# Optimization experiments

Measured on AMD Instinct MI355X. Metric: run time of the kernel, lower is better.

## Reference

```python
import jax, jax.numpy as jnp
import numpy as np

IM = 128  # imSize
BZ = 32


def setup_inputs() -> dict:
    key = jax.random.key(0)
    k1, k2 = jax.random.split(key)
    return {
        "input": jax.random.normal(k1, (BZ, 2, IM, IM), dtype=jnp.float32),
        "mask": jax.random.uniform(k2, (BZ, 1, 1, IM), dtype=jnp.float32),  # unused by forward (as in the torch code)
    }


def _kspace_map(x):
    # x: [B, H, W] real image.
    # Torch pipeline: K = FFT2(x) (unnormalized, torch.rfft onesided=False);
    # for each column i, zero out all k-space columns except i, then IFFT2
    # (normalized=False -> includes 1/(H*W)) and keep the real part.
    # Because each masked spectrum has a single nonzero column, IFFT2 factors:
    #   sep[b,i,u,v] = (1/W) * Re( t[b,u,i] * exp(2j*pi*i*v/W) ),
    # where t = IFFT_rows(K) (includes 1/H). Same math, no (B*W,H,W) FFTs.
    B, H, W = x.shape
    K = jnp.fft.fft2(x)                      # [B,H,W] complex, unnormalized fwd FFT
    t = jnp.fft.ifft(K, axis=1)              # ifft over rows -> carries the 1/H factor
    tt = jnp.transpose(t, (0, 2, 1))         # [B, i(col), u]
    v = jnp.arange(W, dtype=x.dtype)
    ang = (2.0 * np.pi / W) * (v[:, None] * v[None, :])   # [i, v]
    cos_t, sin_t = jnp.cos(ang), jnp.sin(ang)
    # Re(t * e^{j*ang}) = Re(t)*cos - Im(t)*sin  (avoids a large complex temp)
    sep = (tt.real[:, :, :, None] * cos_t[:, None, :]
           - tt.imag[:, :, :, None] * sin_t[:, None, :]) / W   # [B, W, H, W]
    return sep.astype(x.dtype)


def reference(input, mask):
    x = input[:, 0, :, :]          # first channel -> image used for k-space map
    others = input[:, 1:, :, :]    # remaining channels passed through
    sep = _kspace_map(x)           # [B, imSize, H, W]
    return jnp.concatenate([sep, others], axis=1)
```

## Files before the change

kernel.cpp:

```cpp
#include <hip/hip_runtime.h>
#include <math.h>

#define IM 128
#define BZ 32

typedef float v4f __attribute__((ext_vector_type(4)));

__global__ __launch_bounds__(256) void kspace_kernel(const float* __restrict__ in,
                                                     float* __restrict__ out) {
    const int row = blockIdx.x;
    const int b   = row >> 7;
    const int h   = row & (IM - 1);
    const int tid = threadIdx.x;

    const float A = 6.28318530717958647692f / (float)IM;

    __shared__ float xr[IM];
    __shared__ float tre[IM];
    __shared__ float tim[IM];

    const float* xrow = in + (((size_t)b * 2 + 0) * IM + h) * IM;
    if (tid < IM) xr[tid] = xrow[tid];
    __syncthreads();

    {
        const int v     = tid >> 1;
        const int part  = tid & 1;
        const int wbase = part << 6;

        float pc, ps;
        { int k = (v * wbase) & (IM - 1); sincosf(A * (float)k, &ps, &pc); ps = -ps; }
        float rc, rs;
        sincosf(A * (float)v, &rs, &rc); rs = -rs;

        float sre = 0.0f, sim = 0.0f;
        #pragma unroll 8
        for (int i = 0; i < 64; ++i) {
            const float xv = xr[wbase + i];
            sre = fmaf(xv, pc, sre);
            sim = fmaf(xv, ps, sim);
            const float npc = pc * rc - ps * rs;
            ps = fmaf(ps, rc, pc * rs);
            pc = npc;
        }
        sre += __shfl_xor(sre, 1);
        sim += __shfl_xor(sim, 1);
        if (part == 0) {
            tre[v] = sre * (1.0f / IM);
            tim[v] = sim * (1.0f / IM);
        }
    }
    __syncthreads();

    float* outb = out + (size_t)b * 129 * IM * IM + (size_t)h * IM;
    const int vsub = tid >> 5;
    const int w0   = (tid & 31) * 4;

    float pc, ps;
    { int k = (vsub * w0) & (IM - 1); sincosf(A * (float)k, &ps, &pc); }
    float rc, rs;
    sincosf(A * (float)vsub, &rs, &rc);
    float wc, ws;
    { int k = (8 * w0) & (IM - 1); sincosf(A * (float)k, &ws, &wc); }
    const float sc = 0.92387953251128675613f;
    const float ss = 0.38268343236508977173f;

    #pragma unroll
    for (int it = 0; it < 16; ++it) {
        const int v = it * 8 + vsub;
        const float re = tre[v];
        const float im = tim[v];

        v4f r;
        float c = pc, s = ps;
        r.x = re * c - im * s;
        float nc = c * rc - s * rs; s = fmaf(s, rc, c * rs); c = nc;
        r.y = re * c - im * s;
        nc = c * rc - s * rs; s = fmaf(s, rc, c * rs); c = nc;
        r.z = re * c - im * s;
        nc = c * rc - s * rs; s = fmaf(s, rc, c * rs); c = nc;
        r.w = re * c - im * s;
        *(v4f*)(outb + (size_t)v * IM * IM + w0) = r;

        nc = pc * wc - ps * ws; ps = fmaf(ps, wc, pc * ws); pc = nc;
        nc = rc * sc - rs * ss; rs = fmaf(rs, sc, rc * ss); rc = nc;
    }

    if (tid < 32) {
        const v4f* src = (const v4f*)(in + (((size_t)b * 2 + 1) * IM + h) * IM);
        v4f*       dst = (v4f*)(out + (((size_t)b * 129 + 128) * IM + h) * IM);
        dst[tid] = src[tid];
    }
}

extern "C" void kernel_launch(void* const* d_in, const int* in_sizes, int n_in,
                              void* d_out, int out_size, void* d_ws, size_t ws_size,
                              hipStream_t stream) {
    const float* in = (const float*)d_in[0];
    float* out = (float*)d_out;
    kspace_kernel<<<dim3(BZ * IM), dim3(256), 0, stream>>>(in, out);
}
```

Baseline: 273.9 us.

## Split into DFT and emit kernels, staging row DFT results in output buffer

Splits the single kernel in two. The first computes the per-row DFT and stages the real and imaginary parts in the first two rows of each output plane. The second launches one block per (column plane, batch), reads the staged values and writes the whole contiguous 64KB plane using a shared-memory twiddle table instead of recurrences. The goal is contiguous large writes per block in place of scattered 512B row writes, at the cost of a second launch and an extra global round trip. The emit kernel overwrites the staging rows it reads, which is safe only because all threads load them into shared memory before the barrier.

```diff
diff --git a/kernel.cpp b/kernel.cpp
--- a/kernel.cpp
+++ b/kernel.cpp
@@ -6,9 +6,11 @@
 
 typedef float v4f __attribute__((ext_vector_type(4)));
 
-__global__ __launch_bounds__(256) void kspace_kernel(const float* __restrict__ in,
-                                                     float* __restrict__ out) {
-    const int row = blockIdx.x;
+
+__global__ __launch_bounds__(256) void dft_kernel(const float* __restrict__ in,
+                                                  float* __restrict__ out) {
+    const int g   = blockIdx.x;
+    const int row = (g & 7) * (BZ * IM / 8) + (g >> 3);
     const int b   = row >> 7;
     const int h   = row & (IM - 1);
     const int tid = threadIdx.x;
@@ -16,80 +18,86 @@
     const float A = 6.28318530717958647692f / (float)IM;
 
     __shared__ float xr[IM];
-    __shared__ float tre[IM];
-    __shared__ float tim[IM];
-
     const float* xrow = in + (((size_t)b * 2 + 0) * IM + h) * IM;
     if (tid < IM) xr[tid] = xrow[tid];
     __syncthreads();
 
-    {
-        const int v     = tid >> 1;
-        const int part  = tid & 1;
-        const int wbase = part << 6;
+    const int v     = tid >> 1;
+    const int part  = tid & 1;
+    const int wbase = part << 6;
 
-        float pc, ps;
-        { int k = (v * wbase) & (IM - 1); sincosf(A * (float)k, &ps, &pc); ps = -ps; }
-        float rc, rs;
-        sincosf(A * (float)v, &rs, &rc); rs = -rs;
+    float pc, ps;
+    { int k = (v * wbase) & (IM - 1); sincosf(A * (float)k, &ps, &pc); ps = -ps; }
+    float rc, rs;
+    sincosf(A * (float)v, &rs, &rc); rs = -rs;
 
-        float sre = 0.0f, sim = 0.0f;
-        #pragma unroll 8
-        for (int i = 0; i < 64; ++i) {
-            const float xv = xr[wbase + i];
-            sre = fmaf(xv, pc, sre);
-            sim = fmaf(xv, ps, sim);
-            const float npc = pc * rc - ps * rs;
-            ps = fmaf(ps, rc, pc * rs);
-            pc = npc;
-        }
-        sre += __shfl_xor(sre, 1);
-        sim += __shfl_xor(sim, 1);
-        if (part == 0) {
-            tre[v] = sre * (1.0f / IM);
-            tim[v] = sim * (1.0f / IM);
-        }
+    float sre = 0.0f, sim = 0.0f;
+    #pragma unroll 8
+    for (int i = 0; i < 64; ++i) {
+        const float xv = xr[wbase + i];
+        sre = fmaf(xv, pc, sre);
+        sim = fmaf(xv, ps, sim);
+        const float npc = pc * rc - ps * rs;
+        ps = fmaf(ps, rc, pc * rs);
+        pc = npc;
+    }
+    sre += __shfl_xor(sre, 1);
+    sim += __shfl_xor(sim, 1);
+
+    if (part == 0) {
+        float* tb = out + (size_t)(b * 129 + v) * (IM * IM);
+        tb[h]      = sre * (1.0f / IM);
+        tb[IM + h] = sim * (1.0f / IM);
+    }
+}
+
+__global__ __launch_bounds__(256) void emit_kernel(const float* __restrict__ in,
+                                                   float* __restrict__ out) {
+    const int v   = blockIdx.x;
+    const int b   = blockIdx.y;
+    const int tid = threadIdx.x;
+    float* base = out + (size_t)(b * 129 + v) * (IM * IM);
+
+    if (v == IM) {
+        const v4f* src = (const v4f*)(in + ((size_t)b * 2 + 1) * IM * IM);
+        v4f*       dst = (v4f*)base;
+        #pragma unroll
+        for (int it = 0; it < 16; ++it) dst[it * 256 + tid] = src[it * 256 + tid];
+        return;
+    }
+
+    __shared__ float tr[IM], ti[IM], ct[IM], st[IM];
+    const float A = 6.28318530717958647692f / (float)IM;
+    if (tid < IM) {
+        tr[tid] = base[tid];
+        ti[tid] = base[IM + tid];
+        float s, c;
+        sincosf(A * (float)tid, &s, &c);
+        ct[tid] = c; st[tid] = s;
     }
     __syncthreads();
 
-    float* outb = out + (size_t)b * 129 * IM * IM + (size_t)h * IM;
-    const int vsub = tid >> 5;
-    const int w0   = (tid & 31) * 4;
+    const int w0 = (tid & 31) * 4;
+    const int hb = tid >> 5;
 
-    float pc, ps;
-    { int k = (vsub * w0) & (IM - 1); sincosf(A * (float)k, &ps, &pc); }
-    float rc, rs;
-    sincosf(A * (float)vsub, &rs, &rc);
-    float wc, ws;
-    { int k = (8 * w0) & (IM - 1); sincosf(A * (float)k, &ws, &wc); }
-    const float sc = 0.92387953251128675613f;
-    const float ss = 0.38268343236508977173f;
+    float cw[4], sw[4];
+    #pragma unroll
+    for (int j = 0; j < 4; ++j) {
+        const int k = (v * (w0 + j)) & (IM - 1);
+        cw[j] = ct[k]; sw[j] = st[k];
+    }
 
     #pragma unroll
     for (int it = 0; it < 16; ++it) {
-        const int v = it * 8 + vsub;
-        const float re = tre[v];
-        const float im = tim[v];
-
+        const int h  = it * 8 + hb;
+        const float re = tr[h];
+        const float im = ti[h];
         v4f r;
-        float c = pc, s = ps;
-        r.x = re * c - im * s;
-        float nc = c * rc - s * rs; s = fmaf(s, rc, c * rs); c = nc;
-        r.y = re * c - im * s;
-        nc = c * rc - s * rs; s = fmaf(s, rc, c * rs); c = nc;
-        r.z = re * c - im * s;
-        nc = c * rc - s * rs; s = fmaf(s, rc, c * rs); c = nc;
-        r.w = re * c - im * s;
-        *(v4f*)(outb + (size_t)v * IM * IM + w0) = r;
-
-        nc = pc * wc - ps * ws; ps = fmaf(ps, wc, pc * ws); pc = nc;
-        nc = rc * sc - rs * ss; rs = fmaf(rs, sc, rc * ss); rc = nc;
-    }
-
-    if (tid < 32) {
-        const v4f* src = (const v4f*)(in + (((size_t)b * 2 + 1) * IM + h) * IM);
-        v4f*       dst = (v4f*)(out + (((size_t)b * 129 + 128) * IM + h) * IM);
-        dst[tid] = src[tid];
+        r.x = re * cw[0] - im * sw[0];
+        r.y = re * cw[1] - im * sw[1];
+        r.z = re * cw[2] - im * sw[2];
+        r.w = re * cw[3] - im * sw[3];
+        *(v4f*)(base + (size_t)h * IM + w0) = r;
     }
 }
 
@@ -98,5 +106,6 @@
                               hipStream_t stream) {
     const float* in = (const float*)d_in[0];
     float* out = (float*)d_out;
-    kspace_kernel<<<dim3(BZ * IM), dim3(256), 0, stream>>>(in, out);
+    dft_kernel<<<dim3(BZ * IM), dim3(256), 0, stream>>>(in, out);
+    emit_kernel<<<dim3(IM + 1, BZ), dim3(256), 0, stream>>>(in, out);
 }
```

Result: slower. 285.1 us (+4.1%).

## Restructure kernel to tile over output columns with full image in shared memory

Applied to the files above, without the earlier changes.

Each block now loads a whole 128x128 image into XOR-swizzled shared memory and computes the column DFT for 16 output columns, instead of one block per image row. The output phase reads twiddles from a shared cos/sin table rather than advancing them by recurrence, and writes contiguous 128x128 tiles per column. This cuts the grid from 4096 blocks to 256 and uses 64KB of shared memory per block, which limits occupancy. The aim is fewer redundant loads and less trig work, with output still dominated by memory writes.

```diff
diff --git a/kernel.cpp b/kernel.cpp
--- a/kernel.cpp
+++ b/kernel.cpp
@@ -6,90 +6,118 @@
 
 typedef float v4f __attribute__((ext_vector_type(4)));
 
-__global__ __launch_bounds__(256) void kspace_kernel(const float* __restrict__ in,
-                                                     float* __restrict__ out) {
-    const int row = blockIdx.x;
-    const int b   = row >> 7;
-    const int h   = row & (IM - 1);
+
+__global__ __launch_bounds__(256) void kspace_fused(const float* __restrict__ in,
+                                                    float* __restrict__ out) {
+    const int blk = blockIdx.x;
+    const int b   = blk >> 3;
+    const int c   = blk & 7;
     const int tid = threadIdx.x;
 
     const float A = 6.28318530717958647692f / (float)IM;
 
-    __shared__ float xr[IM];
-    __shared__ float tre[IM];
-    __shared__ float tim[IM];
+    __shared__ float xs[IM * IM];
+    __shared__ float ct[IM], st[IM];
 
-    const float* xrow = in + (((size_t)b * 2 + 0) * IM + h) * IM;
-    if (tid < IM) xr[tid] = xrow[tid];
-    __syncthreads();
-
+    const float* xg = in + (size_t)b * 2 * IM * IM;
     {
-        const int v     = tid >> 1;
-        const int part  = tid & 1;
-        const int wbase = part << 6;
-
-        float pc, ps;
-        { int k = (v * wbase) & (IM - 1); sincosf(A * (float)k, &ps, &pc); ps = -ps; }
-        float rc, rs;
-        sincosf(A * (float)v, &rs, &rc); rs = -rs;
-
-        float sre = 0.0f, sim = 0.0f;
-        #pragma unroll 8
-        for (int i = 0; i < 64; ++i) {
-            const float xv = xr[wbase + i];
-            sre = fmaf(xv, pc, sre);
-            sim = fmaf(xv, ps, sim);
-            const float npc = pc * rc - ps * rs;
-            ps = fmaf(ps, rc, pc * rs);
-            pc = npc;
+        const int w  = tid & 127;
+        const int hq = tid >> 7;
+        if (tid < IM) {
+            float s, cc; sincosf(A * (float)tid, &s, &cc);
+            ct[tid] = cc; st[tid] = s;
         }
-        sre += __shfl_xor(sre, 1);
-        sim += __shfl_xor(sim, 1);
-        if (part == 0) {
-            tre[v] = sre * (1.0f / IM);
-            tim[v] = sim * (1.0f / IM);
+        #pragma unroll
+        for (int p = 0; p < 16; ++p) {
+            const int h0 = p * 8 + hq * 4;
+            v4f t;
+            t.x = xg[(h0 + 0) * IM + w];
+            t.y = xg[(h0 + 1) * IM + w];
+            t.z = xg[(h0 + 2) * IM + w];
+            t.w = xg[(h0 + 3) * IM + w];
+            *(v4f*)(xs + w * IM + (h0 ^ ((w & 31) << 2))) = t;
         }
     }
     __syncthreads();
 
-    float* outb = out + (size_t)b * 129 * IM * IM + (size_t)h * IM;
-    const int vsub = tid >> 5;
+    {
+        const int q  = tid >> 5;
+        const int h0 = (tid & 31) * 4;
+        const int va = c * 16 + q;
+        const int vb = va + 8;
+
+        float rc0, rs0, rc1, rs1;
+        sincosf(A * (float)va, &rs0, &rc0); rs0 = -rs0;
+        sincosf(A * (float)vb, &rs1, &rc1); rs1 = -rs1;
+        float pc0 = 1.0f, ps0 = 0.0f, pc1 = 1.0f, ps1 = 0.0f;
+
+        float sre0[4] = {0,0,0,0}, sim0[4] = {0,0,0,0};
+        float sre1[4] = {0,0,0,0}, sim1[4] = {0,0,0,0};
+
+        #pragma unroll 4
+        for (int w = 0; w < IM; ++w) {
+            const v4f xv = *(const v4f*)(xs + w * IM + (h0 ^ ((w & 31) << 2)));
+            sre0[0] = fmaf(xv.x, pc0, sre0[0]); sim0[0] = fmaf(xv.x, ps0, sim0[0]);
+            sre0[1] = fmaf(xv.y, pc0, sre0[1]); sim0[1] = fmaf(xv.y, ps0, sim0[1]);
+            sre0[2] = fmaf(xv.z, pc0, sre0[2]); sim0[2] = fmaf(xv.z, ps0, sim0[2]);
+            sre0[3] = fmaf(xv.w, pc0, sre0[3]); sim0[3] = fmaf(xv.w, ps0, sim0[3]);
+            sre1[0] = fmaf(xv.x, pc1, sre1[0]); sim1[0] = fmaf(xv.x, ps1, sim1[0]);
+            sre1[1] = fmaf(xv.y, pc1, sre1[1]); sim1[1] = fmaf(xv.y, ps1, sim1[1]);
+            sre1[2] = fmaf(xv.z, pc1, sre1[2]); sim1[2] = fmaf(xv.z, ps1, sim1[2]);
+            sre1[3] = fmaf(xv.w, pc1, sre1[3]); sim1[3] = fmaf(xv.w, ps1, sim1[3]);
+            const float n0 = pc0 * rc0 - ps0 * rs0;
+            ps0 = fmaf(ps0, rc0, pc0 * rs0); pc0 = n0;
+            const float n1 = pc1 * rc1 - ps1 * rs1;
+            ps1 = fmaf(ps1, rc1, pc1 * rs1); pc1 = n1;
+        }
+        __syncthreads();
+
+        const float inv = 1.0f / (float)IM;
+        v4f tr0, ti0, tr1, ti1;
+        tr0.x = sre0[0]*inv; tr0.y = sre0[1]*inv; tr0.z = sre0[2]*inv; tr0.w = sre0[3]*inv;
+        ti0.x = sim0[0]*inv; ti0.y = sim0[1]*inv; ti0.z = sim0[2]*inv; ti0.w = sim0[3]*inv;
+        tr1.x = sre1[0]*inv; tr1.y = sre1[1]*inv; tr1.z = sre1[2]*inv; tr1.w = sre1[3]*inv;
+        ti1.x = sim1[0]*inv; ti1.y = sim1[1]*inv; ti1.z = sim1[2]*inv; ti1.w = sim1[3]*inv;
+        *(v4f*)(xs +        q      * IM + h0) = tr0;
+        *(v4f*)(xs + 2048 + q      * IM + h0) = ti0;
+        *(v4f*)(xs +        (q+8)  * IM + h0) = tr1;
+        *(v4f*)(xs + 2048 + (q+8)  * IM + h0) = ti1;
+    }
+    __syncthreads();
+
     const int w0   = (tid & 31) * 4;
+    const int hsub = tid >> 5;
+    float* tiles = out + ((size_t)b * 129 + c * 16) * (IM * IM);
 
-    float pc, ps;
-    { int k = (vsub * w0) & (IM - 1); sincosf(A * (float)k, &ps, &pc); }
-    float rc, rs;
-    sincosf(A * (float)vsub, &rs, &rc);
-    float wc, ws;
-    { int k = (8 * w0) & (IM - 1); sincosf(A * (float)k, &ws, &wc); }
-    const float sc = 0.92387953251128675613f;
-    const float ss = 0.38268343236508977173f;
-
-    #pragma unroll
-    for (int it = 0; it < 16; ++it) {
-        const int v = it * 8 + vsub;
-        const float re = tre[v];
-        const float im = tim[v];
-
-        v4f r;
-        float c = pc, s = ps;
-        r.x = re * c - im * s;
-        float nc = c * rc - s * rs; s = fmaf(s, rc, c * rs); c = nc;
-        r.y = re * c - im * s;
-        nc = c * rc - s * rs; s = fmaf(s, rc, c * rs); c = nc;
-        r.z = re * c - im * s;
-        nc = c * rc - s * rs; s = fmaf(s, rc, c * rs); c = nc;
-        r.w = re * c - im * s;
-        *(v4f*)(outb + (size_t)v * IM * IM + w0) = r;
-
-        nc = pc * wc - ps * ws; ps = fmaf(ps, wc, pc * ws); pc = nc;
-        nc = rc * sc - rs * ss; rs = fmaf(rs, sc, rc * ss); rc = nc;
+    for (int vt = 0; vt < 16; ++vt) {
+        const int v = c * 16 + vt;
+        int k = (v * w0) & (IM - 1);
+        const float cw0 = ct[k], sw0 = st[k]; k = (k + v) & (IM - 1);
+        const float cw1 = ct[k], sw1 = st[k]; k = (k + v) & (IM - 1);
+        const float cw2 = ct[k], sw2 = st[k]; k = (k + v) & (IM - 1);
+        const float cw3 = ct[k], sw3 = st[k];
+        float* tb = tiles + (size_t)vt * (IM * IM);
+        const float* trw = xs + vt * IM;
+        const float* tiw = xs + 2048 + vt * IM;
+        #pragma unroll
+        for (int i = 0; i < 16; ++i) {
+            const int h = i * 8 + hsub;
+            const float re = trw[h];
+            const float im = tiw[h];
+            v4f r;
+            r.x = re * cw0 - im * sw0;
+            r.y = re * cw1 - im * sw1;
+            r.z = re * cw2 - im * sw2;
+            r.w = re * cw3 - im * sw3;
+            *(v4f*)(tb + h * IM + w0) = r;
+        }
     }
 
-    if (tid < 32) {
-        const v4f* src = (const v4f*)(in + (((size_t)b * 2 + 1) * IM + h) * IM);
-        v4f*       dst = (v4f*)(out + (((size_t)b * 129 + 128) * IM + h) * IM);
-        dst[tid] = src[tid];
+    {
+        const v4f* src = (const v4f*)(in + ((size_t)b * 2 + 1) * IM * IM + c * 16 * IM);
+        v4f*       dst = (v4f*)(out + ((size_t)b * 129 + 128) * IM * IM + c * 16 * IM);
+        dst[tid]       = src[tid];
+        dst[256 + tid] = src[256 + tid];
     }
 }
 
@@ -98,5 +126,5 @@
                               hipStream_t stream) {
     const float* in = (const float*)d_in[0];
     float* out = (float*)d_out;
-    kspace_kernel<<<dim3(BZ * IM), dim3(256), 0, stream>>>(in, out);
+    kspace_fused<<<dim3(BZ * 8), dim3(256), 0, stream>>>(in, out);
 }
```

Result: no change. 268.9 us (-1.8%).
